# Kernel tuning notes

Hardware: AMD Instinct MI355X
Metric: run time of the kernel (lower is better)

## Reference

```python
import jax, jax.numpy as jnp
import numpy as np


def setup_inputs() -> dict:
    key = jax.random.key(0)
    k1, k2 = jax.random.split(key)
    shape = (8, 16, 6, 256, 256)  # (n1, n2, band_num, h, w)
    inputs = jax.random.normal(k1, shape, dtype=jnp.float32)
    targets = jax.random.normal(k2, shape, dtype=jnp.float32)
    return {"inputs": inputs, "targets": targets}


def reference(inputs, targets):
    n1, n2, band_num, h, w = inputs.shape
    # Flatten to (n*band_num, h*w): each row is one band of one sample.
    x = inputs.reshape(n1 * n2 * band_num, h * w)
    y = targets.reshape(n1 * n2 * band_num, h * w)
    # torch.var uses unbiased estimator (ddof=1)
    vx = jnp.var(x, axis=1, ddof=1)
    vy = jnp.var(y, axis=1, ddof=1)
    vxy = jnp.var(x + y, axis=1, ddof=1)
    # r = 1 - 0.5*(Var(x+y) - Var(x) - Var(y)) / sqrt(|Var(x)*Var(y)|)
    r = 1.0 - 0.5 * (vxy - vx - vy) / jnp.sqrt(jnp.abs(vx * vy))
    return jnp.mean(r)
```

## Files before the change

kernel.cpp:

```cpp
#include <hip/hip_runtime.h>


#define ROWS 768
#define ROW_ELEMS 65536
#define BLOCK 256
#define SPLIT 4
#define NBLK (ROWS * SPLIT)
#define CHUNK_VECS (ROW_ELEMS / 4 / SPLIT)

typedef float f4 __attribute__((ext_vector_type(4)));

__global__ __launch_bounds__(BLOCK, 4) void partial_kernel(const float* __restrict__ x,
                                                           const float* __restrict__ y,
                                                           float* __restrict__ part) {
    const int blk = blockIdx.x;
    const size_t base = (size_t)blk * (ROW_ELEMS / SPLIT);
    const f4* __restrict__ x4 = (const f4*)(x + base);
    const f4* __restrict__ y4 = (const f4*)(y + base);
    const int tid = threadIdx.x;

    f4 vsx = {0.f, 0.f, 0.f, 0.f};
    f4 vsy = {0.f, 0.f, 0.f, 0.f};
    f4 vsxx = {0.f, 0.f, 0.f, 0.f};
    f4 vsyy = {0.f, 0.f, 0.f, 0.f};
    f4 vsxy = {0.f, 0.f, 0.f, 0.f};

    #pragma unroll
    for (int it = 0; it < 2; ++it) {
        const int i = tid + it * (BLOCK * 8);
        f4 a[8], b[8];
        #pragma unroll
        for (int j = 0; j < 8; ++j)
            a[j] = __builtin_nontemporal_load(&x4[i + j * BLOCK]);
        #pragma unroll
        for (int j = 0; j < 8; ++j)
            b[j] = __builtin_nontemporal_load(&y4[i + j * BLOCK]);
        #pragma unroll
        for (int j = 0; j < 8; ++j) {
            vsx  += a[j];
            vsy  += b[j];
            vsxx += a[j] * a[j];
            vsyy += b[j] * b[j];
            vsxy += a[j] * b[j];
        }
    }

    float sx  = vsx.x  + vsx.y  + vsx.z  + vsx.w;
    float sy  = vsy.x  + vsy.y  + vsy.z  + vsy.w;
    float sxx = vsxx.x + vsxx.y + vsxx.z + vsxx.w;
    float syy = vsyy.x + vsyy.y + vsyy.z + vsyy.w;
    float sxy = vsxy.x + vsxy.y + vsxy.z + vsxy.w;

    #pragma unroll
    for (int off = 32; off > 0; off >>= 1) {
        sx  += __shfl_down(sx,  off);
        sy  += __shfl_down(sy,  off);
        sxx += __shfl_down(sxx, off);
        syy += __shfl_down(syy, off);
        sxy += __shfl_down(sxy, off);
    }

    __shared__ float sm[5][BLOCK / 64];
    const int wave = tid >> 6;
    const int lane = tid & 63;
    if (lane == 0) {
        sm[0][wave] = sx;  sm[1][wave] = sy;
        sm[2][wave] = sxx; sm[3][wave] = syy;
        sm[4][wave] = sxy;
    }
    __syncthreads();

    if (tid == 0) {
        float t0 = 0.f, t1 = 0.f, t2 = 0.f, t3 = 0.f, t4 = 0.f;
        #pragma unroll
        for (int w = 0; w < BLOCK / 64; ++w) {
            t0 += sm[0][w]; t1 += sm[1][w];
            t2 += sm[2][w]; t3 += sm[3][w];
            t4 += sm[4][w];
        }
        part[0 * NBLK + blk] = t0;
        part[1 * NBLK + blk] = t1;
        part[2 * NBLK + blk] = t2;
        part[3 * NBLK + blk] = t3;
        part[4 * NBLK + blk] = t4;
    }
}

__global__ __launch_bounds__(BLOCK) void finalize_kernel(const float* __restrict__ part,
                                                         float* __restrict__ out) {
    float acc = 0.f;
    for (int row = threadIdx.x; row < ROWS; row += BLOCK) {
        float tsx = 0.f, tsy = 0.f, tsxx = 0.f, tsyy = 0.f, tsxy = 0.f;
        #pragma unroll
        for (int c = 0; c < SPLIT; ++c) {
            const int b = row * SPLIT + c;
            tsx  += part[0 * NBLK + b];
            tsy  += part[1 * NBLK + b];
            tsxx += part[2 * NBLK + b];
            tsyy += part[3 * NBLK + b];
            tsxy += part[4 * NBLK + b];
        }
        const float n = (float)ROW_ELEMS;
        const float inv_nm1 = 1.0f / (n - 1.0f);
        float vx  = (tsxx - tsx * tsx / n) * inv_nm1;
        float vy  = (tsyy - tsy * tsy / n) * inv_nm1;
        float cov = (tsxy - tsx * tsy / n) * inv_nm1;
        acc += 1.0f - cov / sqrtf(fabsf(vx * vy));
    }

    #pragma unroll
    for (int off = 32; off > 0; off >>= 1) acc += __shfl_down(acc, off);

    __shared__ float sm[BLOCK / 64];
    const int wave = threadIdx.x >> 6;
    const int lane = threadIdx.x & 63;
    if (lane == 0) sm[wave] = acc;
    __syncthreads();

    if (threadIdx.x == 0) {
        float t = 0.f;
        #pragma unroll
        for (int w = 0; w < BLOCK / 64; ++w) t += sm[w];
        out[0] = t / (float)ROWS;
    }
}

extern "C" void kernel_launch(void* const* d_in, const int* in_sizes, int n_in,
                              void* d_out, int out_size, void* d_ws, size_t ws_size,
                              hipStream_t stream) {
    const float* x = (const float*)d_in[0];
    const float* y = (const float*)d_in[1];
    float* part = (float*)d_ws;
    float* out = (float*)d_out;

    partial_kernel<<<NBLK, BLOCK, 0, stream>>>(x, y, part);
    finalize_kernel<<<1, BLOCK, 0, stream>>>(part, out);
}
```

Baseline: 356.1 us.

## Stream partial sums through a 4-stage LDS pipeline using global_load_lds

Replaces the direct nontemporal register loads with asynchronous global-to-LDS loads into a 4-deep ring buffer of 512-f4 tiles per input. Each tile is consumed from LDS while later tiles are in flight, synchronised with explicit vmcnt waits and barriers. The aim is to keep more memory requests outstanding and hide load latency. In exchange it adds 64 KB of LDS per block, which limits occupancy, plus two barriers per step. It also drops the nontemporal hint and the launch-bounds occupancy hint.

```diff
diff --git a/kernel.cpp b/kernel.cpp
--- a/kernel.cpp
+++ b/kernel.cpp
@@ -6,18 +6,24 @@
 #define BLOCK 256
 #define SPLIT 4
 #define NBLK (ROWS * SPLIT)
-#define CHUNK_VECS (ROW_ELEMS / 4 / SPLIT)
+#define CHUNK_F4 4096
+#define TILE_F4 512
 
 typedef float f4 __attribute__((ext_vector_type(4)));
 
-__global__ __launch_bounds__(BLOCK, 4) void partial_kernel(const float* __restrict__ x,
-                                                           const float* __restrict__ y,
-                                                           float* __restrict__ part) {
+__global__ __launch_bounds__(BLOCK) void partial_kernel(const float* __restrict__ x,
+                                                        const float* __restrict__ y,
+                                                        float* __restrict__ part) {
     const int blk = blockIdx.x;
     const size_t base = (size_t)blk * (ROW_ELEMS / SPLIT);
     const f4* __restrict__ x4 = (const f4*)(x + base);
     const f4* __restrict__ y4 = (const f4*)(y + base);
     const int tid = threadIdx.x;
+    const int w = tid >> 6;
+    const int l = tid & 63;
+
+    __shared__ f4 ldsx[4][TILE_F4];
+    __shared__ f4 ldsy[4][TILE_F4];
 
     f4 vsx = {0.f, 0.f, 0.f, 0.f};
     f4 vsy = {0.f, 0.f, 0.f, 0.f};
@@ -25,25 +31,62 @@
     f4 vsyy = {0.f, 0.f, 0.f, 0.f};
     f4 vsxy = {0.f, 0.f, 0.f, 0.f};
 
-    #pragma unroll
-    for (int it = 0; it < 2; ++it) {
-        const int i = tid + it * (BLOCK * 8);
-        f4 a[8], b[8];
-        #pragma unroll
-        for (int j = 0; j < 8; ++j)
-            a[j] = __builtin_nontemporal_load(&x4[i + j * BLOCK]);
-        #pragma unroll
-        for (int j = 0; j < 8; ++j)
-            b[j] = __builtin_nontemporal_load(&y4[i + j * BLOCK]);
-        #pragma unroll
-        for (int j = 0; j < 8; ++j) {
-            vsx  += a[j];
-            vsy  += b[j];
-            vsxx += a[j] * a[j];
-            vsyy += b[j] * b[j];
-            vsxy += a[j] * b[j];
-        }
+    #define STAGE(t, s)                                                          \
+    {                                                                            \
+        _Pragma("unroll")                                                        \
+        for (int q = 0; q < 2; ++q) {                                            \
+            const f4* sxp = x4 + (t) * TILE_F4 + q * 256 + w * 64 + l;           \
+            const f4* syp = y4 + (t) * TILE_F4 + q * 256 + w * 64 + l;           \
+            __builtin_amdgcn_global_load_lds(                                    \
+                (const __attribute__((address_space(1))) unsigned int*)sxp,      \
+                (__attribute__((address_space(3))) unsigned int*)&ldsx[s][q * 256 + w * 64], \
+                16, 0, 0);                                                       \
+            __builtin_amdgcn_global_load_lds(                                    \
+                (const __attribute__((address_space(1))) unsigned int*)syp,      \
+                (__attribute__((address_space(3))) unsigned int*)&ldsy[s][q * 256 + w * 64], \
+                16, 0, 0);                                                       \
+        }                                                                        \
     }
+
+    #define CONSUME(t, s)                                                        \
+    {                                                                            \
+        _Pragma("unroll")                                                        \
+        for (int jj = 0; jj < 2; ++jj) {                                         \
+            f4 a = ldsx[s][tid + jj * 256];                                      \
+            f4 b = ldsy[s][tid + jj * 256];                                      \
+            vsx += a; vsy += b;                                                  \
+            vsxx += a * a; vsyy += b * b; vsxy += a * b;                         \
+        }                                                                        \
+    }
+
+    #define STEP(t, vm, STAGE_STMT)                                              \
+    {                                                                            \
+        STAGE_STMT;                                                              \
+        asm volatile("s_waitcnt vmcnt(" #vm ")" ::: "memory");                   \
+        __builtin_amdgcn_s_barrier();                                            \
+        __builtin_amdgcn_sched_barrier(0);                                       \
+        CONSUME(t, (t) & 3);                                                     \
+        asm volatile("s_waitcnt lgkmcnt(0)" ::: "memory");                       \
+        __builtin_amdgcn_sched_barrier(0);                                       \
+        __builtin_amdgcn_s_barrier();                                            \
+    }
+
+    STAGE(0, 0);
+    STAGE(1, 1);
+    STAGE(2, 2);
+
+    STEP(0, 12, STAGE(3, 3));
+    STEP(1, 12, STAGE(4, 0));
+    STEP(2, 12, STAGE(5, 1));
+    STEP(3, 12, STAGE(6, 2));
+    STEP(4, 12, STAGE(7, 3));
+    STEP(5, 8, );
+    STEP(6, 4, );
+    STEP(7, 0, );
+
+    #undef STEP
+    #undef CONSUME
+    #undef STAGE
 
     float sx  = vsx.x  + vsx.y  + vsx.z  + vsx.w;
     float sy  = vsy.x  + vsy.y  + vsy.z  + vsy.w;
@@ -61,22 +104,20 @@
     }
 
     __shared__ float sm[5][BLOCK / 64];
-    const int wave = tid >> 6;
-    const int lane = tid & 63;
-    if (lane == 0) {
-        sm[0][wave] = sx;  sm[1][wave] = sy;
-        sm[2][wave] = sxx; sm[3][wave] = syy;
-        sm[4][wave] = sxy;
+    if (l == 0) {
+        sm[0][w] = sx;  sm[1][w] = sy;
+        sm[2][w] = sxx; sm[3][w] = syy;
+        sm[4][w] = sxy;
     }
     __syncthreads();
 
     if (tid == 0) {
         float t0 = 0.f, t1 = 0.f, t2 = 0.f, t3 = 0.f, t4 = 0.f;
         #pragma unroll
-        for (int w = 0; w < BLOCK / 64; ++w) {
-            t0 += sm[0][w]; t1 += sm[1][w];
-            t2 += sm[2][w]; t3 += sm[3][w];
-            t4 += sm[4][w];
+        for (int ww = 0; ww < BLOCK / 64; ++ww) {
+            t0 += sm[0][ww]; t1 += sm[1][ww];
+            t2 += sm[2][ww]; t3 += sm[3][ww];
+            t4 += sm[4][ww];
         }
         part[0 * NBLK + blk] = t0;
         part[1 * NBLK + blk] = t1;
```

Result: slower. 395.1 us (+11.0%).
